# Kernel optimization log

Measured on AMD Instinct MI355X. Metric: run time of the kernel, lower is better.

## Reference

```python
import jax, jax.numpy as jnp
import numpy as np

N_NODES = 100000
N_EDGES = 1250000
IN_DIM = 64
HID_DIM = 64
OUT_DIM = 64
NEG_SLOPE = 0.2
EPS = 1e-16  # PyG softmax denominator epsilon


def _xavier(key, shape):
    fan_in, fan_out = shape[1], shape[0]
    lim = jnp.sqrt(6.0 / (fan_in + fan_out))
    return jax.random.uniform(key, shape, jnp.float32, -lim, lim)


def setup_inputs() -> dict:
    key = jax.random.key(0)
    ks = jax.random.split(key, 10)
    x = jax.random.normal(ks[0], (N_NODES, IN_DIM), jnp.float32)
    edge_index = jax.random.randint(ks[1], (2, N_EDGES), 0, N_NODES, jnp.int64)
    edge_attr = jax.random.uniform(ks[2], (N_EDGES,), jnp.float32)
    # layer 1 params (torch Linear weight layout: [out, in])
    W1 = _xavier(ks[3], (HID_DIM, IN_DIM))
    a_src1 = _xavier(ks[4], (1, HID_DIM))[0]
    a_dst1 = _xavier(ks[5], (1, HID_DIM))[0]
    # layer 2 params
    W2 = _xavier(ks[6], (OUT_DIM, HID_DIM))
    a_src2 = _xavier(ks[7], (1, OUT_DIM))[0]
    a_dst2 = _xavier(ks[8], (1, OUT_DIM))[0]
    return {"x": x, "edge_index": edge_index, "edge_attr": edge_attr,
            "W1": W1, "a_src1": a_src1, "a_dst1": a_dst1,
            "W2": W2, "a_src2": a_src2, "a_dst2": a_dst2}


def gat_layer(x, W, a_src, a_dst, src, dst, edge_weight, num_nodes):
    # linear (no bias): h = x @ W^T, h: [N, out]
    h = x @ W.T
    s_src = h @ a_src  # [N]
    s_dst = h @ a_dst  # [N]
    # per-edge raw score; note j = edge_index[0] (src), i = edge_index[1] (dst)
    alpha = s_src[src] + s_dst[dst]  # [E]
    alpha = jnp.where(alpha >= 0, alpha, NEG_SLOPE * alpha)  # leaky_relu
    # segment softmax over destination nodes
    seg_max = jax.ops.segment_max(alpha, dst, num_segments=num_nodes)
    alpha = jnp.exp(alpha - seg_max[dst])
    seg_sum = jax.ops.segment_sum(alpha, dst, num_segments=num_nodes)
    alpha = alpha / (seg_sum[dst] + EPS)
    alpha = alpha * edge_weight
    # weighted scatter-add aggregation of source features
    msg = h[src] * alpha[:, None]  # [E, out]
    return jax.ops.segment_sum(msg, dst, num_segments=num_nodes)


def reference(x, edge_index, edge_attr, W1, a_src1, a_dst1, W2, a_src2, a_dst2):
    src = edge_index[0]
    dst = edge_index[1]
    h = gat_layer(x, W1, a_src1, a_dst1, src, dst, edge_attr, N_NODES)
    h = jax.nn.relu(h)
    out = gat_layer(h, W2, a_src2, a_dst2, src, dst, edge_attr, N_NODES)
    return out
```

## Files before the change

### kernel.cpp

```cpp
#include <hip/hip_runtime.h>

#define NN 100000
#define NE 1250000
#define DIM 64

#define BSHIFT 9
#define BNODES (1 << BSHIFT)
#define NBUCK ((NN + BNODES - 1) / BNODES)
#define BIN_BLOCKS 512
#define BIN_CHUNK ((NE + BIN_BLOCKS - 1) / BIN_BLOCKS)

typedef unsigned short bf16_t;
typedef __attribute__((ext_vector_type(8))) short short8;
typedef __attribute__((ext_vector_type(8))) unsigned short ushort8;
typedef __attribute__((ext_vector_type(4))) float f32x4;

static __device__ __forceinline__ bf16_t f2bf(float f) {
    union { float f; unsigned int u; } c; c.f = f;
    unsigned int u = c.u;
    u += 0x7FFFu + ((u >> 16) & 1u);
    return (bf16_t)(u >> 16);
}
static __device__ __forceinline__ float bf2f(bf16_t b) {
    union { unsigned int u; float f; } c; c.u = ((unsigned int)b) << 16;
    return c.f;
}

union ABFrag { short8 v; short s[8]; };

template<bool IN_BF16, bool RELU_IN>
static __device__ __forceinline__
void linear_body(int bid, const void* __restrict__ xin,
                 const float* __restrict__ W,
                 const float* __restrict__ a_src,
                 const float* __restrict__ a_dst,
                 bf16_t* __restrict__ h,
                 float* __restrict__ s_src,
                 float* __restrict__ s_dst)
{
    int tid  = threadIdx.x;
    int lane = tid & 63;
    int wid  = tid >> 6;
    int lr   = lane & 15;
    int lg   = lane >> 4;
    int rowbase = bid * 64 + wid * 16;

    ABFrag Bf[4][2];
#pragma unroll
    for (int t = 0; t < 4; ++t)
#pragma unroll
    for (int s = 0; s < 2; ++s) {
        const f32x4* wp = reinterpret_cast<const f32x4*>(W + (lr + 16*t)*DIM + 32*s + 8*lg);
        f32x4 w0 = wp[0], w1 = wp[1];
#pragma unroll
        for (int j = 0; j < 4; ++j) {
            Bf[t][s].s[j]     = (short)f2bf(w0[j]);
            Bf[t][s].s[j + 4] = (short)f2bf(w1[j]);
        }
    }

    int arow = rowbase + lr;
    if (arow > NN - 1) arow = NN - 1;

    ABFrag Af[2];
    if (IN_BF16) {
        const bf16_t* xp = (const bf16_t*)xin + (size_t)arow * DIM + 8*lg;
#pragma unroll
        for (int s = 0; s < 2; ++s) {
            ushort8 xv = *reinterpret_cast<const ushort8*>(xp + 32*s);
#pragma unroll
            for (int j = 0; j < 8; ++j) {
                unsigned short b = xv[j];
                if (RELU_IN) b = (b & 0x8000u) ? (unsigned short)0 : b;
                Af[s].s[j] = (short)b;
            }
        }
    } else {
        const float* xp = (const float*)xin + (size_t)arow * DIM + 8*lg;
#pragma unroll
        for (int s = 0; s < 2; ++s) {
            const f32x4* xq = reinterpret_cast<const f32x4*>(xp + 32*s);
            f32x4 x0 = xq[0], x1 = xq[1];
#pragma unroll
            for (int j = 0; j < 4; ++j) {
                float f0 = x0[j], f1 = x1[j];
                if (RELU_IN) { f0 = f0 > 0.f ? f0 : 0.f; f1 = f1 > 0.f ? f1 : 0.f; }
                Af[s].s[j]     = (short)f2bf(f0);
                Af[s].s[j + 4] = (short)f2bf(f1);
            }
        }
    }

    f32x4 acc[4] = {{0.f,0.f,0.f,0.f},{0.f,0.f,0.f,0.f},{0.f,0.f,0.f,0.f},{0.f,0.f,0.f,0.f}};
#pragma unroll
    for (int s = 0; s < 2; ++s)
#pragma unroll
    for (int t = 0; t < 4; ++t)
        acc[t] = __builtin_amdgcn_mfma_f32_16x16x32_bf16(Af[s].v, Bf[t][s].v, acc[t], 0, 0, 0);

    float av[4], dv[4];
#pragma unroll
    for (int t = 0; t < 4; ++t) { av[t] = a_src[lr + 16*t]; dv[t] = a_dst[lr + 16*t]; }

    float ssv[4], sdv[4];
#pragma unroll
    for (int r = 0; r < 4; ++r) {
        int row = rowbase + 4*lg + r;
        bool ok = row < NN;
        float ps = 0.f, pd = 0.f;
#pragma unroll
        for (int t = 0; t < 4; ++t) {
            float v = acc[t][r];
            ps += v * av[t];
            pd += v * dv[t];
            if (ok) h[(size_t)row * DIM + lr + 16*t] = f2bf(v);
        }
#pragma unroll
        for (int off = 8; off; off >>= 1) {
            ps += __shfl_xor(ps, off, 64);
            pd += __shfl_xor(pd, off, 64);
        }
        ssv[r] = ps; sdv[r] = pd;
    }
    if (lr == 0) {
#pragma unroll
        for (int r = 0; r < 4; ++r) {
            int row = rowbase + 4*lg + r;
            if (row < NN) { s_src[row] = ssv[r]; s_dst[row] = sdv[r]; }
        }
    }
}

__global__ __launch_bounds__(256)
void bin_hist(const int* __restrict__ dst, int* __restrict__ gcnt)
{
    __shared__ int cnt[NBUCK];
    int tid = threadIdx.x;
    for (int i = tid; i < NBUCK; i += 256) cnt[i] = 0;
    __syncthreads();
    int lo = blockIdx.x * BIN_CHUNK;
    int hi = lo + BIN_CHUNK; if (hi > NE) hi = NE;
    for (int e = lo + tid; e < hi; e += 256)
        atomicAdd(&cnt[dst[e] >> BSHIFT], 1);
    __syncthreads();
    for (int i = tid; i < NBUCK; i += 256)
        gcnt[i * BIN_BLOCKS + blockIdx.x] = cnt[i];
}

__global__ __launch_bounds__(512)
void row_scan(int* __restrict__ gcnt, int* __restrict__ btot)
{
    __shared__ int wpart[8];
    int b    = blockIdx.x;
    int tid  = threadIdx.x;
    int lane = tid & 63;
    int v = gcnt[b * BIN_BLOCKS + tid];
    int sc = v;
#pragma unroll
    for (int off = 1; off <= 32; off <<= 1) {
        int t = __shfl_up(sc, off, 64);
        if (lane >= off) sc += t;
    }
    if (lane == 63) wpart[tid >> 6] = sc;
    __syncthreads();
    if (tid == 0) {
        int run = 0;
#pragma unroll
        for (int k = 0; k < 8; ++k) { int t = wpart[k]; wpart[k] = run; run += t; }
    }
    __syncthreads();
    int incl = sc + wpart[tid >> 6];
    gcnt[b * BIN_BLOCKS + tid] = incl - v;
    if (tid == BIN_BLOCKS - 1) btot[b] = incl;
}

__global__ __launch_bounds__(256)
void bucket_scan(const int* __restrict__ btot, int* __restrict__ bbase,
                 int* __restrict__ rowptr)
{
    __shared__ int s[NBUCK];
    int tid = threadIdx.x;
    if (tid < NBUCK) s[tid] = btot[tid];
    __syncthreads();
    if (tid == 0) {
        int run = 0;
        for (int i = 0; i < NBUCK; ++i) { int t = s[i]; s[i] = run; run += t; }
        rowptr[NN] = NE;
    }
    __syncthreads();
    if (tid < NBUCK) bbase[tid] = s[tid];
}

__global__ __launch_bounds__(256)
void scatter_linear1(const int* __restrict__ src, const int* __restrict__ dst,
                     const float* __restrict__ ea,
                     const int* __restrict__ gcnt, const int* __restrict__ bbase,
                     int2* __restrict__ region,
                     const float* __restrict__ x, const float* __restrict__ W1,
                     const float* __restrict__ as1, const float* __restrict__ ad1,
                     bf16_t* __restrict__ h,
                     float* __restrict__ ssrc, float* __restrict__ sdst)
{
    if (blockIdx.x < BIN_BLOCKS) {
        __shared__ int cur[NBUCK];
        int tid = threadIdx.x;
        for (int i = tid; i < NBUCK; i += 256)
            cur[i] = gcnt[i * BIN_BLOCKS + blockIdx.x] + bbase[i];
        __syncthreads();
        int lo = blockIdx.x * BIN_CHUNK;
        int hi = lo + BIN_CHUNK; if (hi > NE) hi = NE;
        for (int e = lo + tid; e < hi; e += 256) {
            int d = dst[e];
            int b = d >> BSHIFT;
            int pos = atomicAdd(&cur[b], 1);
            region[pos] = make_int2(src[e] | ((d & (BNODES - 1)) << 17),
                                    __float_as_int(ea[e]));
        }
    } else {
        linear_body<false, false>(blockIdx.x - BIN_BLOCKS, x, W1, as1, ad1, h, ssrc, sdst);
    }
}

__global__ __launch_bounds__(256)
void linear2(const void* __restrict__ xin, const float* __restrict__ W,
             const float* __restrict__ a_src, const float* __restrict__ a_dst,
             bf16_t* __restrict__ h, float* __restrict__ s_src, float* __restrict__ s_dst)
{
    linear_body<true, true>(blockIdx.x, xin, W, a_src, a_dst, h, s_src, s_dst);
}

__global__ __launch_bounds__(512)
void build_csr(const int* __restrict__ btot, const int* __restrict__ bbase,
               const int2* __restrict__ region,
               int* __restrict__ rowptr, int2* __restrict__ csr)
{
    int b    = blockIdx.x;
    int tid  = threadIdx.x;
    int lane = tid & 63;
    int cnt  = btot[b];
    int base = bbase[b];
    const int2* rec = region + base;

    __shared__ int ncnt[BNODES];
    __shared__ int curs[BNODES];
    __shared__ int wpart[8];
    ncnt[tid] = 0;
    __syncthreads();
    for (int i = tid; i < cnt; i += 512)
        atomicAdd(&ncnt[(rec[i].x >> 17) & (BNODES - 1)], 1);
    __syncthreads();

    int v = ncnt[tid];
    int sc = v;
#pragma unroll
    for (int off = 1; off <= 32; off <<= 1) {
        int t = __shfl_up(sc, off, 64);
        if (lane >= off) sc += t;
    }
    if (lane == 63) wpart[tid >> 6] = sc;
    __syncthreads();
    if (tid == 0) {
        int run = 0;
#pragma unroll
        for (int k = 0; k < 8; ++k) { int t = wpart[k]; wpart[k] = run; run += t; }
    }
    __syncthreads();
    int excl = sc - v + wpart[tid >> 6];

    int node = (b << BSHIFT) + tid;
    if (node < NN) rowptr[node] = base + excl;
    curs[tid] = base + excl;
    __syncthreads();

    for (int i = tid; i < cnt; i += 512) {
        int2 r = rec[i];
        int dl = (r.x >> 17) & (BNODES - 1);
        int pos = atomicAdd(&curs[dl], 1);
        csr[pos] = make_int2(r.x & 0x1FFFF, r.y);
    }
}

template<bool OUT_BF16>
__global__ __launch_bounds__(256)
void fused_agg(const int* __restrict__ rowptr,
               const int2* __restrict__ csr,
               const float* __restrict__ ssrc, const float* __restrict__ sdst,
               const bf16_t* __restrict__ h,
               void* __restrict__ outp)
{
    int tid  = threadIdx.x;
    int lane = tid & 63;
    int wv   = tid >> 6;
    int grp  = lane >> 4;
    int lr   = lane & 15;
    int d    = blockIdx.x * 16 + wv * 4 + grp;
    bool dok = d < NN;

    int rb = 0, deg = 0;
    if (dok) { rb = rowptr[d]; deg = rowptr[d + 1] - rb; }
    float sdd = dok ? sdst[d] : 0.f;

    int wmax = deg;
    wmax = max(wmax, __shfl_xor(wmax, 16, 64));
    wmax = max(wmax, __shfl_xor(wmax, 32, 64));

    float psum = 0.f;
    float ax = 0.f, ay = 0.f, az = 0.f, aw = 0.f;

#define GSWZ(J)                                                                 \
    int   sj##J = __builtin_amdgcn_ds_swizzle(s, (((J) << 5) | 0x10));          \
    float wj##J = __int_as_float(__builtin_amdgcn_ds_swizzle(wbits, (((J) << 5) | 0x10)));
#define GLOAD(J)                                                                \
    ushort4 hv##J = *reinterpret_cast<const ushort4*>(h + (size_t)sj##J * DIM + 4*lr);
#define GACC(J)                                                                 \
    ax += wj##J * bf2f(hv##J.x); ay += wj##J * bf2f(hv##J.y);                   \
    az += wj##J * bf2f(hv##J.z); aw += wj##J * bf2f(hv##J.w);

    for (int cb = 0; cb < wmax; cb += 16) {
        int idx = cb + lr;
        bool v = idx < deg;
        int2 rec = v ? csr[rb + idx] : make_int2(0, 0);
        int   s  = rec.x;
        float a  = ssrc[s] + sdd;
        a = (a >= 0.f) ? a : 0.2f * a;
        a = fminf(a, 60.f);
        float p = v ? __expf(a) : 0.f;
        float w = p * __int_as_float(rec.y);
        int wbits = __float_as_int(w);

        GSWZ(0)  GSWZ(1)  GSWZ(2)  GSWZ(3)  GSWZ(4)  GSWZ(5)  GSWZ(6)  GSWZ(7)
        GSWZ(8)  GSWZ(9)  GSWZ(10) GSWZ(11) GSWZ(12) GSWZ(13) GSWZ(14) GSWZ(15)
        GLOAD(0)  GLOAD(1)  GLOAD(2)  GLOAD(3)  GLOAD(4)  GLOAD(5)  GLOAD(6)  GLOAD(7)
        GLOAD(8)  GLOAD(9)  GLOAD(10) GLOAD(11) GLOAD(12) GLOAD(13) GLOAD(14) GLOAD(15)

        float ps = p;
#pragma unroll
        for (int off = 1; off <= 8; off <<= 1) ps += __shfl_xor(ps, off, 64);
        psum += ps;

        GACC(0)  GACC(1)  GACC(2)  GACC(3)  GACC(4)  GACC(5)  GACC(6)  GACC(7)
        GACC(8)  GACC(9)  GACC(10) GACC(11) GACC(12) GACC(13) GACC(14) GACC(15)
    }
#undef GSWZ
#undef GLOAD
#undef GACC

    if (dok) {
        float inv = 1.f / (psum + 1e-16f);
        if (OUT_BF16) {
            ushort4 o;
            o.x = f2bf(ax * inv); o.y = f2bf(ay * inv);
            o.z = f2bf(az * inv); o.w = f2bf(aw * inv);
            *reinterpret_cast<ushort4*>((bf16_t*)outp + (size_t)d * DIM + 4*lr) = o;
        } else {
            float4 o = make_float4(ax * inv, ay * inv, az * inv, aw * inv);
            *reinterpret_cast<float4*>((float*)outp + (size_t)d * DIM + 4*lr) = o;
        }
    }
}

extern "C" void kernel_launch(void* const* d_in, const int* in_sizes, int n_in,
                              void* d_out, int out_size, void* d_ws, size_t ws_size,
                              hipStream_t stream) {
    const float* x   = (const float*)d_in[0];
    const int*   ei  = (const int*)d_in[1];
    const float* ea  = (const float*)d_in[2];
    const float* W1  = (const float*)d_in[3];
    const float* as1 = (const float*)d_in[4];
    const float* ad1 = (const float*)d_in[5];
    const float* W2  = (const float*)d_in[6];
    const float* as2 = (const float*)d_in[7];
    const float* ad2 = (const float*)d_in[8];
    const int* src = ei;
    const int* dst = ei + NE;
    float* out = (float*)d_out;

    char* p = (char*)d_ws;
    auto carve = [&](size_t bytes) { char* r = p; p += (bytes + 255) & ~(size_t)255; return (void*)r; };
    bf16_t*  acc_bf = (bf16_t*)carve((size_t)NN * DIM * 2);
    bf16_t*  h      = (bf16_t*)carve((size_t)NN * DIM * 2);
    float*   ssrc   = (float*)carve((size_t)NN * 4);
    float*   sdst   = (float*)carve((size_t)NN * 4);
    int*     rowptr = (int*)carve((size_t)(NN + 1) * 4);
    int2*    csr    = (int2*)carve((size_t)NE * 8);
    int2*    region = (int2*)carve((size_t)NE * 8);
    int*     gcnt   = (int*)carve((size_t)NBUCK * BIN_BLOCKS * 4);
    int*     bbase  = (int*)carve((size_t)NBUCK * 4);
    int*     btot   = (int*)carve((size_t)NBUCK * 4);

    const int GRID_LIN  = (NN + 63) / 64;
    const int GRID_NODE = (NN + 15) / 16;

    bin_hist<<<BIN_BLOCKS, 256, 0, stream>>>(dst, gcnt);
    row_scan<<<NBUCK, BIN_BLOCKS, 0, stream>>>(gcnt, btot);
    bucket_scan<<<1, 256, 0, stream>>>(btot, bbase, rowptr);
    scatter_linear1<<<BIN_BLOCKS + GRID_LIN, 256, 0, stream>>>(
        src, dst, ea, gcnt, bbase, region, x, W1, as1, ad1, h, ssrc, sdst);
    build_csr<<<NBUCK, 512, 0, stream>>>(btot, bbase, region, rowptr, csr);

    fused_agg<true><<<GRID_NODE, 256, 0, stream>>>(rowptr, csr, ssrc, sdst, h, acc_bf);

    linear2<<<GRID_LIN, 256, 0, stream>>>(acc_bf, W2, as2, ad2, h, ssrc, sdst);
    fused_agg<false><<<GRID_NODE, 256, 0, stream>>>(rowptr, csr, ssrc, sdst, h, out);
}
```

Baseline: 132.6 us.

## Use fixed-capacity buckets to drop bucket_scan and switch to row end pointers

Each destination bucket gets a fixed-capacity slot in region and csr (BCAP entries per 256-node bucket). This removes the serial single-block bucket_scan launch, and fused_agg reads degree from a separate rend array instead of rowptr[d+1]. Bucket size, histogram block count and block sizes for the binning, linear and CSR kernels are retuned to match. Correctness now depends on no bucket exceeding BCAP edges, which holds for uniform random graphs (about 3200 edges per bucket) but would overflow on skewed inputs.

```diff
diff --git a/kernel.cpp b/kernel.cpp
--- a/kernel.cpp
+++ b/kernel.cpp
@@ -4,11 +4,12 @@
 #define NE 1250000
 #define DIM 64
 
-#define BSHIFT 9
+#define BSHIFT 8
 #define BNODES (1 << BSHIFT)
 #define NBUCK ((NN + BNODES - 1) / BNODES)
-#define BIN_BLOCKS 512
+#define BIN_BLOCKS 256
 #define BIN_CHUNK ((NE + BIN_BLOCKS - 1) / BIN_BLOCKS)
+#define BCAP 4096
 
 typedef unsigned short bf16_t;
 typedef __attribute__((ext_vector_type(8))) short short8;
@@ -43,7 +44,7 @@
     int wid  = tid >> 6;
     int lr   = lane & 15;
     int lg   = lane >> 4;
-    int rowbase = bid * 64 + wid * 16;
+    int rowbase = bid * 128 + wid * 16;
 
     ABFrag Bf[4][2];
 #pragma unroll
@@ -131,26 +132,26 @@
     }
 }
 
-__global__ __launch_bounds__(256)
+__global__ __launch_bounds__(512)
 void bin_hist(const int* __restrict__ dst, int* __restrict__ gcnt)
 {
     __shared__ int cnt[NBUCK];
     int tid = threadIdx.x;
-    for (int i = tid; i < NBUCK; i += 256) cnt[i] = 0;
+    for (int i = tid; i < NBUCK; i += 512) cnt[i] = 0;
     __syncthreads();
     int lo = blockIdx.x * BIN_CHUNK;
     int hi = lo + BIN_CHUNK; if (hi > NE) hi = NE;
-    for (int e = lo + tid; e < hi; e += 256)
+    for (int e = lo + tid; e < hi; e += 512)
         atomicAdd(&cnt[dst[e] >> BSHIFT], 1);
     __syncthreads();
-    for (int i = tid; i < NBUCK; i += 256)
+    for (int i = tid; i < NBUCK; i += 512)
         gcnt[i * BIN_BLOCKS + blockIdx.x] = cnt[i];
 }
 
-__global__ __launch_bounds__(512)
+__global__ __launch_bounds__(256)
 void row_scan(int* __restrict__ gcnt, int* __restrict__ btot)
 {
-    __shared__ int wpart[8];
+    __shared__ int wpart[4];
     int b    = blockIdx.x;
     int tid  = threadIdx.x;
     int lane = tid & 63;
@@ -166,7 +167,7 @@
     if (tid == 0) {
         int run = 0;
 #pragma unroll
-        for (int k = 0; k < 8; ++k) { int t = wpart[k]; wpart[k] = run; run += t; }
+        for (int k = 0; k < 4; ++k) { int t = wpart[k]; wpart[k] = run; run += t; }
     }
     __syncthreads();
     int incl = sc + wpart[tid >> 6];
@@ -174,27 +175,10 @@
     if (tid == BIN_BLOCKS - 1) btot[b] = incl;
 }
 
-__global__ __launch_bounds__(256)
-void bucket_scan(const int* __restrict__ btot, int* __restrict__ bbase,
-                 int* __restrict__ rowptr)
-{
-    __shared__ int s[NBUCK];
-    int tid = threadIdx.x;
-    if (tid < NBUCK) s[tid] = btot[tid];
-    __syncthreads();
-    if (tid == 0) {
-        int run = 0;
-        for (int i = 0; i < NBUCK; ++i) { int t = s[i]; s[i] = run; run += t; }
-        rowptr[NN] = NE;
-    }
-    __syncthreads();
-    if (tid < NBUCK) bbase[tid] = s[tid];
-}
-
-__global__ __launch_bounds__(256)
+__global__ __launch_bounds__(512)
 void scatter_linear1(const int* __restrict__ src, const int* __restrict__ dst,
                      const float* __restrict__ ea,
-                     const int* __restrict__ gcnt, const int* __restrict__ bbase,
+                     const int* __restrict__ gcnt,
                      int2* __restrict__ region,
                      const float* __restrict__ x, const float* __restrict__ W1,
                      const float* __restrict__ as1, const float* __restrict__ ad1,
@@ -204,12 +188,12 @@
     if (blockIdx.x < BIN_BLOCKS) {
         __shared__ int cur[NBUCK];
         int tid = threadIdx.x;
-        for (int i = tid; i < NBUCK; i += 256)
-            cur[i] = gcnt[i * BIN_BLOCKS + blockIdx.x] + bbase[i];
+        for (int i = tid; i < NBUCK; i += 512)
+            cur[i] = gcnt[i * BIN_BLOCKS + blockIdx.x] + i * BCAP;
         __syncthreads();
         int lo = blockIdx.x * BIN_CHUNK;
         int hi = lo + BIN_CHUNK; if (hi > NE) hi = NE;
-        for (int e = lo + tid; e < hi; e += 256) {
+        for (int e = lo + tid; e < hi; e += 512) {
             int d = dst[e];
             int b = d >> BSHIFT;
             int pos = atomicAdd(&cur[b], 1);
@@ -221,7 +205,7 @@
     }
 }
 
-__global__ __launch_bounds__(256)
+__global__ __launch_bounds__(512)
 void linear2(const void* __restrict__ xin, const float* __restrict__ W,
              const float* __restrict__ a_src, const float* __restrict__ a_dst,
              bf16_t* __restrict__ h, float* __restrict__ s_src, float* __restrict__ s_dst)
@@ -229,24 +213,24 @@
     linear_body<true, true>(blockIdx.x, xin, W, a_src, a_dst, h, s_src, s_dst);
 }
 
-__global__ __launch_bounds__(512)
-void build_csr(const int* __restrict__ btot, const int* __restrict__ bbase,
+__global__ __launch_bounds__(256)
+void build_csr(const int* __restrict__ btot,
                const int2* __restrict__ region,
-               int* __restrict__ rowptr, int2* __restrict__ csr)
+               int* __restrict__ rowptr, int* __restrict__ rend,
+               int2* __restrict__ csr)
 {
     int b    = blockIdx.x;
     int tid  = threadIdx.x;
     int lane = tid & 63;
     int cnt  = btot[b];
-    int base = bbase[b];
-    const int2* rec = region + base;
+    const int2* rec = region + (size_t)b * BCAP;
 
     __shared__ int ncnt[BNODES];
     __shared__ int curs[BNODES];
-    __shared__ int wpart[8];
+    __shared__ int wpart[4];
     ncnt[tid] = 0;
     __syncthreads();
-    for (int i = tid; i < cnt; i += 512)
+    for (int i = tid; i < cnt; i += 256)
         atomicAdd(&ncnt[(rec[i].x >> 17) & (BNODES - 1)], 1);
     __syncthreads();
 
@@ -262,17 +246,18 @@
     if (tid == 0) {
         int run = 0;
 #pragma unroll
-        for (int k = 0; k < 8; ++k) { int t = wpart[k]; wpart[k] = run; run += t; }
+        for (int k = 0; k < 4; ++k) { int t = wpart[k]; wpart[k] = run; run += t; }
     }
     __syncthreads();
     int excl = sc - v + wpart[tid >> 6];
+    int base = b * BCAP;
 
     int node = (b << BSHIFT) + tid;
-    if (node < NN) rowptr[node] = base + excl;
+    if (node < NN) { rowptr[node] = base + excl; rend[node] = base + excl + v; }
     curs[tid] = base + excl;
     __syncthreads();
 
-    for (int i = tid; i < cnt; i += 512) {
+    for (int i = tid; i < cnt; i += 256) {
         int2 r = rec[i];
         int dl = (r.x >> 17) & (BNODES - 1);
         int pos = atomicAdd(&curs[dl], 1);
@@ -282,7 +267,7 @@
 
 template<bool OUT_BF16>
 __global__ __launch_bounds__(256)
-void fused_agg(const int* __restrict__ rowptr,
+void fused_agg(const int* __restrict__ rowptr, const int* __restrict__ rend,
                const int2* __restrict__ csr,
                const float* __restrict__ ssrc, const float* __restrict__ sdst,
                const bf16_t* __restrict__ h,
@@ -297,7 +282,7 @@
     bool dok = d < NN;
 
     int rb = 0, deg = 0;
-    if (dok) { rb = rowptr[d]; deg = rowptr[d + 1] - rb; }
+    if (dok) { rb = rowptr[d]; deg = rend[d] - rb; }
     float sdd = dok ? sdst[d] : 0.f;
 
     int wmax = deg;
@@ -381,25 +366,24 @@
     bf16_t*  h      = (bf16_t*)carve((size_t)NN * DIM * 2);
     float*   ssrc   = (float*)carve((size_t)NN * 4);
     float*   sdst   = (float*)carve((size_t)NN * 4);
-    int*     rowptr = (int*)carve((size_t)(NN + 1) * 4);
-    int2*    csr    = (int2*)carve((size_t)NE * 8);
-    int2*    region = (int2*)carve((size_t)NE * 8);
+    int*     rowptr = (int*)carve((size_t)NN * 4);
+    int*     rend   = (int*)carve((size_t)NN * 4);
+    int2*    csr    = (int2*)carve((size_t)NBUCK * BCAP * 8);
+    int2*    region = (int2*)carve((size_t)NBUCK * BCAP * 8);
     int*     gcnt   = (int*)carve((size_t)NBUCK * BIN_BLOCKS * 4);
-    int*     bbase  = (int*)carve((size_t)NBUCK * 4);
     int*     btot   = (int*)carve((size_t)NBUCK * 4);
 
-    const int GRID_LIN  = (NN + 63) / 64;
+    const int GRID_LIN  = (NN + 127) / 128;
     const int GRID_NODE = (NN + 15) / 16;
 
-    bin_hist<<<BIN_BLOCKS, 256, 0, stream>>>(dst, gcnt);
-    row_scan<<<NBUCK, BIN_BLOCKS, 0, stream>>>(gcnt, btot);
-    bucket_scan<<<1, 256, 0, stream>>>(btot, bbase, rowptr);
-    scatter_linear1<<<BIN_BLOCKS + GRID_LIN, 256, 0, stream>>>(
-        src, dst, ea, gcnt, bbase, region, x, W1, as1, ad1, h, ssrc, sdst);
-    build_csr<<<NBUCK, 512, 0, stream>>>(btot, bbase, region, rowptr, csr);
-
-    fused_agg<true><<<GRID_NODE, 256, 0, stream>>>(rowptr, csr, ssrc, sdst, h, acc_bf);
-
-    linear2<<<GRID_LIN, 256, 0, stream>>>(acc_bf, W2, as2, ad2, h, ssrc, sdst);
-    fused_agg<false><<<GRID_NODE, 256, 0, stream>>>(rowptr, csr, ssrc, sdst, h, out);
-}
+    bin_hist<<<BIN_BLOCKS, 512, 0, stream>>>(dst, gcnt);
+    row_scan<<<NBUCK, 256, 0, stream>>>(gcnt, btot);
+    scatter_linear1<<<BIN_BLOCKS + GRID_LIN, 512, 0, stream>>>(
+        src, dst, ea, gcnt, region, x, W1, as1, ad1, h, ssrc, sdst);
+    build_csr<<<NBUCK, 256, 0, stream>>>(btot, region, rowptr, rend, csr);
+
+    fused_agg<true><<<GRID_NODE, 256, 0, stream>>>(rowptr, rend, csr, ssrc, sdst, h, acc_bf);
+
+    linear2<<<GRID_LIN, 512, 0, stream>>>(acc_bf, W2, as2, ad2, h, ssrc, sdst);
+    fused_agg<false><<<GRID_NODE, 256, 0, stream>>>(rowptr, rend, csr, ssrc, sdst, h, out);
+}
```

New measurement: 133.8 us. About the same (+0.9%).
